# Performance work log

Hardware: AMD Instinct MI355X
Metric: run time of the kernel (lower is better)

The kernel has to match this reference:

```python
import jax, jax.numpy as jnp
import numpy as np

LAMDA = 0.001


def setup_inputs() -> dict:
    key = jax.random.key(0)
    k1, k2 = jax.random.split(key)
    embeddings = jax.random.normal(k1, (256, 1, 256, 256), dtype=jnp.float32)
    labels = jax.random.randint(k2, (256,), 0, 8, dtype=jnp.int64)
    return {"embeddings": embeddings, "labels": labels, "epoch": 1}


def _offdiag(M, b):
    # Remove the diagonal of a (b, b) matrix -> (b, b-1), same trick as torch code:
    # flatten()[1:].view(b-1, b+1)[:, :-1].reshape(b, b-1)
    return M.reshape(-1)[1:].reshape(b - 1, b + 1)[:, :-1].reshape(b, b - 1)


def _psd(embeddings):
    x = embeddings[:, 0]                      # (b, h, w), requires c == 1
    h, w = x.shape[1], x.shape[2]
    k = h * w
    dft = jnp.fft.fft2(x)                     # (b, h, w) complex
    avgpsd = jnp.mean((dft * jnp.conj(dft)).real, axis=0)   # (h, w)
    # log of (geometric mean / arithmetic mean) style flatness measure
    return jnp.clip(jnp.sum(jnp.log(avgpsd)) / k - jnp.log(jnp.sum(avgpsd) / k), 0.0, 100.0)


def reference(embeddings, labels, epoch):
    b = embeddings.shape[0]
    loss = -LAMDA * epoch * _psd(embeddings)

    e = embeddings.reshape(b, -1)             # (b, d)
    sq = jnp.sum(e * e, axis=1)               # (b,)
    d2 = sq[:, None] + sq[None, :] - 2.0 * (e @ e.T)   # squared pairwise distances
    d2 = jnp.maximum(d2, 0.0)
    D = jnp.where(d2 > 0, jnp.sqrt(jnp.where(d2 > 0, d2, 1.0)), 0.0)  # safe sqrt

    Doff = _offdiag(D, b)                     # (b, b-1)
    sm = jax.nn.softmax(-Doff, axis=1)        # (b, b-1)

    Loff = _offdiag(jnp.broadcast_to(labels[None, :], (b, b)), b)  # labels[j != i]
    mask = Loff == labels[:, None]            # positives per row
    probs = jnp.sum(jnp.where(mask, sm, 0.0), axis=1)  # (b,)

    loss = loss + jnp.sum(-jnp.log(probs)) / 200.0
    return loss
```

## Files before the change

kernel.cpp:

```cpp
#include <hip/hip_runtime.h>
#include <hip/hip_bf16.h>
#include <math.h>

#define NROW 256
#define DIM  65536
#define KB   256
#define LR   264
#define PSP  65600

typedef __attribute__((ext_vector_type(8))) short short8;
typedef __attribute__((ext_vector_type(4))) float f32x4;
typedef unsigned int       u32t;
typedef unsigned long long u64t;

__device__ __forceinline__ float bf2f(ushort h) {
    u32t u = ((u32t)h) << 16;
    return __builtin_bit_cast(float, u);
}
__device__ __forceinline__ u32t pk2(float lo, float hi) {
    __hip_bfloat162 h = __float22bfloat162_rn(make_float2(lo, hi));
    u32t r; __builtin_memcpy(&r, &h, 4); return r;
}

__device__ __forceinline__ int gpos(int i, int j) {
    const int wid  = ((i >> 7) << 2) | (j >> 6);
    const int lane = (((i >> 2) & 3) << 4) | (j & 15);
    const int m = (i >> 4) & 7, n = (j >> 4) & 3, jr = i & 3;
    return ((wid << 6) | lane) * 128 + (((m << 2) | n) << 2) + jr;
}

__global__ __launch_bounds__(512) void gemm_fused(const float* __restrict__ E,
                                                  ushort* __restrict__ part) {
    const int s    = blockIdx.x;
    const int tid  = threadIdx.x;
    const int lane = tid & 63;
    const int wid  = tid >> 6;
    const int r15  = lane & 15;
    const int kgi  = lane >> 4;

    __shared__ ushort Es[NROW][LR];

    const int r8   = lane >> 3;
    const int g    = lane & 7;
    const int rowb = wid * 32 + r8;
    const float* __restrict__ gb = E + ((size_t)rowb << 16)
                                     + (size_t)s * KB + (size_t)g * 4;

    float4 v[32];
    #pragma unroll
    for (int c = 0; c < 4; ++c)
        #pragma unroll
        for (int u = 0; u < 8; ++u)
            v[c * 8 + u] = *(const float4*)(gb + ((size_t)(c * 8) << 16) + u * 32);

    #pragma unroll
    for (int c = 0; c < 4; ++c)
        #pragma unroll
        for (int u = 0; u < 8; ++u) {
            const int row = rowb + c * 8;
            uint2 wv;
            wv.x = pk2(v[c * 8 + u].x, v[c * 8 + u].y);
            wv.y = pk2(v[c * 8 + u].z, v[c * 8 + u].w);
            *(uint2*)&Es[row][u * 32 + g * 4] = wv;
        }

    __syncthreads();

    const int wr = wid >> 2;
    const int wc = wid & 3;

    f32x4 acc[8][4];
    #pragma unroll
    for (int m = 0; m < 8; ++m)
        #pragma unroll
        for (int n = 0; n < 4; ++n) acc[m][n] = (f32x4){0.f, 0.f, 0.f, 0.f};

    #pragma unroll
    for (int kk = 0; kk < 8; ++kk) {
        const int ko = kk * 32 + kgi * 8;
        short8 af[8], bfr[4];
        #pragma unroll
        for (int m = 0; m < 8; ++m)
            af[m] = *(const short8*)&Es[wr * 128 + m * 16 + r15][ko];
        #pragma unroll
        for (int n = 0; n < 4; ++n)
            bfr[n] = *(const short8*)&Es[wc * 64 + n * 16 + r15][ko];
        #pragma unroll
        for (int m = 0; m < 8; ++m)
            #pragma unroll
            for (int n = 0; n < 4; ++n)
                acc[m][n] = __builtin_amdgcn_mfma_f32_16x16x32_bf16(
                    af[m], bfr[n], acc[m][n], 0, 0, 0);
    }

    ushort* pp = part + (size_t)s * PSP + (size_t)tid * 128;
    #pragma unroll
    for (int m = 0; m < 8; ++m)
        #pragma unroll
        for (int n = 0; n < 4; n += 2) {
            uint4 q;
            q.x = pk2(acc[m][n][0],     acc[m][n][1]);
            q.y = pk2(acc[m][n][2],     acc[m][n][3]);
            q.z = pk2(acc[m][n + 1][0], acc[m][n + 1][1]);
            q.w = pk2(acc[m][n + 1][2], acc[m][n + 1][3]);
            *(uint4*)(pp + ((m << 2) | n) * 4) = q;
        }
}

__global__ __launch_bounds__(256) void reduce_k(const ushort* __restrict__ part,
                                                float* __restrict__ Gh,
                                                u64t* __restrict__ acc,
                                                u32t* __restrict__ cnt) {
    if (blockIdx.x == 0 && threadIdx.x == 0) { *acc = 0ull; *cnt = 0u; }

    const int b = blockIdx.x & 255;
    const int h = blockIdx.x >> 8;
    const int t = threadIdx.x, l = t & 63, sg = t >> 6;
    const int n0 = b * 256 + l * 4;

    const ushort* base = part + (size_t)(h * 128 + sg) * PSP + n0;

    uint2 r[32];
    #pragma unroll
    for (int u = 0; u < 32; ++u)
        r[u] = *(const uint2*)(base + (size_t)(4 * u) * PSP);

    float a0 = 0.f, a1 = 0.f, a2 = 0.f, a3 = 0.f;
    #pragma unroll
    for (int u = 0; u < 32; ++u) {
        a0 += bf2f((ushort)(r[u].x & 0xffffu));
        a1 += bf2f((ushort)(r[u].x >> 16));
        a2 += bf2f((ushort)(r[u].y & 0xffffu));
        a3 += bf2f((ushort)(r[u].y >> 16));
    }
    __shared__ float sh[4][256];
    sh[sg][l * 4 + 0] = a0; sh[sg][l * 4 + 1] = a1;
    sh[sg][l * 4 + 2] = a2; sh[sg][l * 4 + 3] = a3;
    __syncthreads();
    Gh[(size_t)h * 65536 + b * 256 + t] =
        (sh[0][t] + sh[1][t]) + (sh[2][t] + sh[3][t]);
}

__global__ __launch_bounds__(256) void row_loss_k(const float* __restrict__ Gh,
                                                  const int* __restrict__ labels,
                                                  u64t* __restrict__ acc,
                                                  u32t* __restrict__ cnt,
                                                  float* __restrict__ out) {
    const int i = blockIdx.x;
    const int j = threadIdx.x;

    const int pii = gpos(i, i), pjj = gpos(j, j), pij = gpos(i, j);
    const float Gii = Gh[pii] + Gh[65536 + pii];
    const float Gjj = Gh[pjj] + Gh[65536 + pjj];
    const float Gij = Gh[pij] + Gh[65536 + pij];
    const float d2 = fmaxf(Gii + Gjj - 2.0f * Gij, 0.0f);
    const bool diag = (j == i);
    const float sc = diag ? -3.0e38f : -sqrtf(d2);

    __shared__ float red0[4], red1[4];

    float m = sc;
    #pragma unroll
    for (int off = 32; off; off >>= 1) m = fmaxf(m, __shfl_xor(m, off, 64));
    const int w = j >> 6;
    if ((j & 63) == 0) red0[w] = m;
    __syncthreads();
    m = fmaxf(fmaxf(red0[0], red0[1]), fmaxf(red0[2], red0[3]));

    const float p  = diag ? 0.0f : expf(sc - m);
    const float nm = (labels[j] == labels[i]) ? p : 0.0f;

    float zs = p, ns = nm;
    #pragma unroll
    for (int off = 32; off; off >>= 1) {
        zs += __shfl_xor(zs, off, 64);
        ns += __shfl_xor(ns, off, 64);
    }
    __syncthreads();
    if ((j & 63) == 0) { red0[w] = zs; red1[w] = ns; }
    __syncthreads();
    if (j == 0) {
        const float Z = red0[0] + red0[1] + red0[2] + red0[3];
        const float N = red1[0] + red1[1] + red1[2] + red1[3];
        const float rl = logf(Z) - logf(N);
        const long long q = llrintf(rl * 1048576.0f);
        atomicAdd(acc, (u64t)q);
        __threadfence();
        const u32t c = atomicAdd(cnt, 1u);
        if (c == NROW - 1) {
            __threadfence();
            const u64t tot = atomicAdd(acc, 0ull);
            out[0] = (float)((double)(long long)tot * (1.0 / 1048576.0) * 0.005);
        }
    }
}

extern "C" void kernel_launch(void* const* d_in, const int* in_sizes, int n_in,
                              void* d_out, int out_size, void* d_ws, size_t ws_size,
                              hipStream_t stream) {
    const float* E      = (const float*)d_in[0];
    const int*   labels = (const int*)d_in[1];
    float*       out    = (float*)d_out;

    ushort* part = (ushort*)d_ws;
    float*  Gh   = (float*)((char*)d_ws + (size_t)256 * PSP * sizeof(ushort));
    u64t*   acc  = (u64t*)(Gh + 2 * NROW * NROW);
    u32t*   cnt  = (u32t*)(acc + 1);

    gemm_fused<<<256, 512, 0, stream>>>(E, part);
    reduce_k  <<<512, 256, 0, stream>>>(part, Gh, acc, cnt);
    row_loss_k<<<NROW, 256, 0, stream>>>(Gh, labels, acc, cnt, out);
}
```

Baseline: 45.40 us.

## Double-buffer K chunks in LDS to overlap global loads with MFMA

The split-K GEMM kernel now loads its 256-wide K slice in four 64-wide chunks into a double-buffered LDS tile. The next chunk's global loads are issued while MFMAs run on the current one, where previously the whole slice was loaded before any compute started. LDS use drops from about 135KB to about 74KB and the launch bounds request 2 blocks per CU, aiming at more latency hiding. The cost is extra barriers, and 128 accumulator registers per thread under the tighter register budget may spill. The grid has only 256 blocks, so the occupancy hint may have little effect.

```diff
diff --git a/kernel.cpp b/kernel.cpp
--- a/kernel.cpp
+++ b/kernel.cpp
@@ -5,7 +5,8 @@
 #define NROW 256
 #define DIM  65536
 #define KB   256
-#define LR   264
+#define CH   64
+#define LSTR 72
 #define PSP  65600
 
 typedef __attribute__((ext_vector_type(8))) short short8;
@@ -29,68 +30,77 @@
     return ((wid << 6) | lane) * 128 + (((m << 2) | n) << 2) + jr;
 }
 
-__global__ __launch_bounds__(512) void gemm_fused(const float* __restrict__ E,
-                                                  ushort* __restrict__ part) {
+__global__ __launch_bounds__(512, 2) void gemm_k(const float* __restrict__ E,
+                                                 ushort* __restrict__ part) {
     const int s    = blockIdx.x;
     const int tid  = threadIdx.x;
     const int lane = tid & 63;
     const int wid  = tid >> 6;
+    const int wr   = wid >> 2;
+    const int wc   = wid & 3;
     const int r15  = lane & 15;
     const int kgi  = lane >> 4;
 
-    __shared__ ushort Es[NROW][LR];
+    __shared__ ushort es[2][NROW][LSTR];
 
     const int r8   = lane >> 3;
     const int g    = lane & 7;
-    const int rowb = wid * 32 + r8;
-    const float* __restrict__ gb = E + ((size_t)rowb << 16)
-                                     + (size_t)s * KB + (size_t)g * 4;
-
-    float4 v[32];
-    #pragma unroll
-    for (int c = 0; c < 4; ++c)
-        #pragma unroll
-        for (int u = 0; u < 8; ++u)
-            v[c * 8 + u] = *(const float4*)(gb + ((size_t)(c * 8) << 16) + u * 32);
-
-    #pragma unroll
-    for (int c = 0; c < 4; ++c)
+    const int rowb = wid * 32;
+    const float* __restrict__ gb = E + (size_t)s * KB;
+
+    f32x4 acc4[8][4];
+    #pragma unroll
+    for (int m = 0; m < 8; ++m)
+        #pragma unroll
+        for (int n = 0; n < 4; ++n) acc4[m][n] = (f32x4){0.f, 0.f, 0.f, 0.f};
+
+    auto LOADC = [&](int c, float4* v) {
         #pragma unroll
         for (int u = 0; u < 8; ++u) {
-            const int row = rowb + c * 8;
+            const int row = rowb + (u & 3) * 8 + r8;
+            const int kf  = (u >> 2) * 32 + g * 4;
+            v[u] = *(const float4*)(gb + ((size_t)row << 16) + c * CH + kf);
+        }
+    };
+    auto WRITEC = [&](int buf, const float4* v) {
+        #pragma unroll
+        for (int u = 0; u < 8; ++u) {
+            const int row = rowb + (u & 3) * 8 + r8;
+            const int kf  = (u >> 2) * 32 + g * 4;
             uint2 wv;
-            wv.x = pk2(v[c * 8 + u].x, v[c * 8 + u].y);
-            wv.y = pk2(v[c * 8 + u].z, v[c * 8 + u].w);
-            *(uint2*)&Es[row][u * 32 + g * 4] = wv;
-        }
-
-    __syncthreads();
-
-    const int wr = wid >> 2;
-    const int wc = wid & 3;
-
-    f32x4 acc[8][4];
-    #pragma unroll
-    for (int m = 0; m < 8; ++m)
-        #pragma unroll
-        for (int n = 0; n < 4; ++n) acc[m][n] = (f32x4){0.f, 0.f, 0.f, 0.f};
-
-    #pragma unroll
-    for (int kk = 0; kk < 8; ++kk) {
-        const int ko = kk * 32 + kgi * 8;
-        short8 af[8], bfr[4];
-        #pragma unroll
-        for (int m = 0; m < 8; ++m)
-            af[m] = *(const short8*)&Es[wr * 128 + m * 16 + r15][ko];
-        #pragma unroll
-        for (int n = 0; n < 4; ++n)
-            bfr[n] = *(const short8*)&Es[wc * 64 + n * 16 + r15][ko];
-        #pragma unroll
-        for (int m = 0; m < 8; ++m)
+            wv.x = pk2(v[u].x, v[u].y);
+            wv.y = pk2(v[u].z, v[u].w);
+            *(uint2*)&es[buf][row][kf] = wv;
+        }
+    };
+
+    float4 v0[8];
+    LOADC(0, v0);
+    WRITEC(0, v0);
+
+    #pragma unroll
+    for (int c = 0; c < 4; ++c) {
+        __syncthreads();
+        float4 vn[8];
+        if (c < 3) LOADC(c + 1, vn);
+        #pragma unroll
+        for (int kk = 0; kk < 2; ++kk) {
+            const int ko = kk * 32 + kgi * 8;
+            short8 af[8], bfr[4];
+            #pragma unroll
+            for (int m = 0; m < 8; ++m)
+                af[m] = *(const short8*)&es[c & 1][wr * 128 + m * 16 + r15][ko];
             #pragma unroll
             for (int n = 0; n < 4; ++n)
-                acc[m][n] = __builtin_amdgcn_mfma_f32_16x16x32_bf16(
-                    af[m], bfr[n], acc[m][n], 0, 0, 0);
+                bfr[n] = *(const short8*)&es[c & 1][wc * 64 + n * 16 + r15][ko];
+            #pragma unroll
+            for (int m = 0; m < 8; ++m)
+                #pragma unroll
+                for (int n = 0; n < 4; ++n)
+                    acc4[m][n] = __builtin_amdgcn_mfma_f32_16x16x32_bf16(
+                        af[m], bfr[n], acc4[m][n], 0, 0, 0);
+        }
+        if (c < 3) WRITEC((c + 1) & 1, vn);
     }
 
     ushort* pp = part + (size_t)s * PSP + (size_t)tid * 128;
@@ -99,10 +109,10 @@
         #pragma unroll
         for (int n = 0; n < 4; n += 2) {
             uint4 q;
-            q.x = pk2(acc[m][n][0],     acc[m][n][1]);
-            q.y = pk2(acc[m][n][2],     acc[m][n][3]);
-            q.z = pk2(acc[m][n + 1][0], acc[m][n + 1][1]);
-            q.w = pk2(acc[m][n + 1][2], acc[m][n + 1][3]);
+            q.x = pk2(acc4[m][n][0],     acc4[m][n][1]);
+            q.y = pk2(acc4[m][n][2],     acc4[m][n][3]);
+            q.z = pk2(acc4[m][n + 1][0], acc4[m][n + 1][1]);
+            q.w = pk2(acc4[m][n + 1][2], acc4[m][n + 1][3]);
             *(uint4*)(pp + ((m << 2) | n) * 4) = q;
         }
 }
@@ -207,7 +217,7 @@
     u64t*   acc  = (u64t*)(Gh + 2 * NROW * NROW);
     u32t*   cnt  = (u32t*)(acc + 1);
 
-    gemm_fused<<<256, 512, 0, stream>>>(E, part);
+    gemm_k    <<<256, 512, 0, stream>>>(E, part);
     reduce_k  <<<512, 256, 0, stream>>>(part, Gh, acc, cnt);
     row_loss_k<<<NROW, 256, 0, stream>>>(Gh, labels, acc, cnt, out);
 }
```

After: 45.74 us. About the same (+0.8%).

## Split GEMM blocks by row half and double-buffer K chunks in shared memory

Applied to the files above, without the earlier changes.

The Gram GEMM now launches 512 blocks, each computing one 128-row half of the output for a 256-wide K slice. Blocks stream that slice through a small double-buffered shared-memory tile in 32-column chunks, so global loads of the next chunk overlap MFMA work on the current one. The smaller accumulator array and smaller LDS footprint are meant to allow more resident blocks per CU (launch bounds of 4). In exchange each half-block reloads the full 256-row B operand, doubling global reads of the embeddings. The partial-sum layout, the reduce indexing and gpos are all updated to match.

```diff
diff --git a/kernel.cpp b/kernel.cpp
--- a/kernel.cpp
+++ b/kernel.cpp
@@ -4,9 +4,8 @@
 
 #define NROW 256
 #define DIM  65536
-#define KB   256
-#define LR   264
-#define PSP  65600
+#define LSTR 40
+#define PSP2 32832
 
 typedef __attribute__((ext_vector_type(8))) short short8;
 typedef __attribute__((ext_vector_type(4))) float f32x4;
@@ -22,80 +21,86 @@
     u32t r; __builtin_memcpy(&r, &h, 4); return r;
 }
 
-__device__ __forceinline__ int gpos(int i, int j) {
-    const int wid  = ((i >> 7) << 2) | (j >> 6);
-    const int lane = (((i >> 2) & 3) << 4) | (j & 15);
-    const int m = (i >> 4) & 7, n = (j >> 4) & 3, jr = i & 3;
-    return ((wid << 6) | lane) * 128 + (((m << 2) | n) << 2) + jr;
-}
-
-__global__ __launch_bounds__(512) void gemm_fused(const float* __restrict__ E,
-                                                  ushort* __restrict__ part) {
-    const int s    = blockIdx.x;
+__device__ __forceinline__ int gpos2(int i, int j) {
+    const int mh  = i >> 7, il = i & 127;
+    const int wid  = ((il >> 6) << 2) | (j >> 6);
+    const int lane = (((il >> 2) & 3) << 4) | (j & 15);
+    const int q = ((wid << 6) | lane) * 64
+                + (((((il >> 4) & 3) << 2) | ((j >> 4) & 3)) << 2) + (il & 3);
+    return mh * 32768 + q;
+}
+
+__global__ __launch_bounds__(512, 4) void gemm_k(const float* __restrict__ E,
+                                                 ushort* __restrict__ part) {
+    const int b   = blockIdx.x;
+    const int x   = b & 7;
+    const int mh  = (b >> 3) & 1;
+    const int s   = x * 32 + (b >> 4);
+
     const int tid  = threadIdx.x;
     const int lane = tid & 63;
     const int wid  = tid >> 6;
+    const int wr   = wid >> 2;
+    const int wc   = wid & 3;
     const int r15  = lane & 15;
     const int kgi  = lane >> 4;
 
-    __shared__ ushort Es[NROW][LR];
-
-    const int r8   = lane >> 3;
-    const int g    = lane & 7;
-    const int rowb = wid * 32 + r8;
-    const float* __restrict__ gb = E + ((size_t)rowb << 16)
-                                     + (size_t)s * KB + (size_t)g * 4;
-
-    float4 v[32];
-    #pragma unroll
-    for (int c = 0; c < 4; ++c)
-        #pragma unroll
-        for (int u = 0; u < 8; ++u)
-            v[c * 8 + u] = *(const float4*)(gb + ((size_t)(c * 8) << 16) + u * 32);
-
-    #pragma unroll
-    for (int c = 0; c < 4; ++c)
-        #pragma unroll
-        for (int u = 0; u < 8; ++u) {
-            const int row = rowb + c * 8;
+    __shared__ ushort es[2][NROW][LSTR];
+
+    const int row  = tid >> 1;
+    const int half = tid & 1;
+    const size_t kbase = (size_t)s * 256;
+
+    f32x4 acc[4][4];
+    #pragma unroll
+    for (int m = 0; m < 4; ++m)
+        #pragma unroll
+        for (int n = 0; n < 4; ++n) acc[m][n] = (f32x4){0.f, 0.f, 0.f, 0.f};
+
+    auto LOADC = [&](int c, float4* v) {
+        const float* p = E + ((size_t)row << 16) + kbase + c * 32 + half * 16;
+        #pragma unroll
+        for (int u = 0; u < 4; ++u) v[u] = *(const float4*)(p + u * 4);
+    };
+    auto WRITEC = [&](int buf, const float4* v) {
+        #pragma unroll
+        for (int u = 0; u < 4; ++u) {
             uint2 wv;
-            wv.x = pk2(v[c * 8 + u].x, v[c * 8 + u].y);
-            wv.y = pk2(v[c * 8 + u].z, v[c * 8 + u].w);
-            *(uint2*)&Es[row][u * 32 + g * 4] = wv;
+            wv.x = pk2(v[u].x, v[u].y);
+            wv.y = pk2(v[u].z, v[u].w);
+            *(uint2*)&es[buf][row][half * 16 + u * 4] = wv;
         }
-
-    __syncthreads();
-
-    const int wr = wid >> 2;
-    const int wc = wid & 3;
-
-    f32x4 acc[8][4];
-    #pragma unroll
-    for (int m = 0; m < 8; ++m)
-        #pragma unroll
-        for (int n = 0; n < 4; ++n) acc[m][n] = (f32x4){0.f, 0.f, 0.f, 0.f};
-
-    #pragma unroll
-    for (int kk = 0; kk < 8; ++kk) {
-        const int ko = kk * 32 + kgi * 8;
-        short8 af[8], bfr[4];
-        #pragma unroll
-        for (int m = 0; m < 8; ++m)
-            af[m] = *(const short8*)&Es[wr * 128 + m * 16 + r15][ko];
+    };
+
+    float4 v0[4];
+    LOADC(0, v0);
+    WRITEC(0, v0);
+
+    #pragma unroll
+    for (int c = 0; c < 8; ++c) {
+        __syncthreads();
+        float4 vn[4];
+        if (c < 7) LOADC(c + 1, vn);
+        const int ko = kgi * 8;
+        short8 af[4], bfr[4];
+        #pragma unroll
+        for (int m = 0; m < 4; ++m)
+            af[m] = *(const short8*)&es[c & 1][mh * 128 + wr * 64 + m * 16 + r15][ko];
         #pragma unroll
         for (int n = 0; n < 4; ++n)
-            bfr[n] = *(const short8*)&Es[wc * 64 + n * 16 + r15][ko];
-        #pragma unroll
-        for (int m = 0; m < 8; ++m)
+            bfr[n] = *(const short8*)&es[c & 1][wc * 64 + n * 16 + r15][ko];
+        #pragma unroll
+        for (int m = 0; m < 4; ++m)
             #pragma unroll
             for (int n = 0; n < 4; ++n)
                 acc[m][n] = __builtin_amdgcn_mfma_f32_16x16x32_bf16(
                     af[m], bfr[n], acc[m][n], 0, 0, 0);
-    }
-
-    ushort* pp = part + (size_t)s * PSP + (size_t)tid * 128;
-    #pragma unroll
-    for (int m = 0; m < 8; ++m)
+        if (c < 7) WRITEC((c + 1) & 1, vn);
+    }
+
+    ushort* pp = part + (size_t)(s * 2 + mh) * PSP2 + (size_t)tid * 64;
+    #pragma unroll
+    for (int m = 0; m < 4; ++m)
         #pragma unroll
         for (int n = 0; n < 4; n += 2) {
             uint4 q;
@@ -113,17 +118,19 @@
                                                 u32t* __restrict__ cnt) {
     if (blockIdx.x == 0 && threadIdx.x == 0) { *acc = 0ull; *cnt = 0u; }
 
-    const int b = blockIdx.x & 255;
-    const int h = blockIdx.x >> 8;
+    const int w  = blockIdx.x & 255;
+    const int h  = blockIdx.x >> 8;
+    const int mh = w >> 7;
+    const int q0 = (w & 127) * 256;
     const int t = threadIdx.x, l = t & 63, sg = t >> 6;
-    const int n0 = b * 256 + l * 4;
-
-    const ushort* base = part + (size_t)(h * 128 + sg) * PSP + n0;
+
+    const ushort* base = part + (size_t)((h * 128 + sg) * 2 + mh) * PSP2
+                              + q0 + l * 4;
 
     uint2 r[32];
     #pragma unroll
     for (int u = 0; u < 32; ++u)
-        r[u] = *(const uint2*)(base + (size_t)(4 * u) * PSP);
+        r[u] = *(const uint2*)(base + (size_t)(8 * u) * PSP2);
 
     float a0 = 0.f, a1 = 0.f, a2 = 0.f, a3 = 0.f;
     #pragma unroll
@@ -137,7 +144,7 @@
     sh[sg][l * 4 + 0] = a0; sh[sg][l * 4 + 1] = a1;
     sh[sg][l * 4 + 2] = a2; sh[sg][l * 4 + 3] = a3;
     __syncthreads();
-    Gh[(size_t)h * 65536 + b * 256 + t] =
+    Gh[(size_t)h * 65536 + w * 256 + t] =
         (sh[0][t] + sh[1][t]) + (sh[2][t] + sh[3][t]);
 }
 
@@ -149,7 +156,7 @@
     const int i = blockIdx.x;
     const int j = threadIdx.x;
 
-    const int pii = gpos(i, i), pjj = gpos(j, j), pij = gpos(i, j);
+    const int pii = gpos2(i, i), pjj = gpos2(j, j), pij = gpos2(i, j);
     const float Gii = Gh[pii] + Gh[65536 + pii];
     const float Gjj = Gh[pjj] + Gh[65536 + pjj];
     const float Gij = Gh[pij] + Gh[65536 + pij];
@@ -203,11 +210,11 @@
     float*       out    = (float*)d_out;
 
     ushort* part = (ushort*)d_ws;
-    float*  Gh   = (float*)((char*)d_ws + (size_t)256 * PSP * sizeof(ushort));
-    u64t*   acc  = (u64t*)(Gh + 2 * NROW * NROW);
+    float*  Gh   = (float*)((char*)d_ws + (size_t)512 * PSP2 * sizeof(ushort));
+    u64t*   acc  = (u64t*)(Gh + 2 * 65536);
     u32t*   cnt  = (u32t*)(acc + 1);
 
-    gemm_fused<<<256, 512, 0, stream>>>(E, part);
+    gemm_k    <<<512, 512, 0, stream>>>(E, part);
     reduce_k  <<<512, 256, 0, stream>>>(part, Gh, acc, cnt);
     row_loss_k<<<NROW, 256, 0, stream>>>(Gh, labels, acc, cnt, out);
 }
```

Measured after the change: 47.30 us. 4.2% more time.
